# Performance work log

Measured on AMD Instinct MI355X. Metric: run time of the kernel, lower is better.

Reference implementation:

```python
import jax, jax.numpy as jnp
import numpy as np

VOCAB = 32000
EMBED = 512
HIDDEN = 512
SEQ = 4096


def setup_inputs() -> dict:
    key = jax.random.key(0)
    ks = jax.random.split(key, 20)
    s = 1.0 / np.sqrt(HIDDEN)

    def n(k, shape):
        return (jax.random.normal(k, shape, dtype=jnp.float32) * s).astype(jnp.float32)

    inp = {}
    inp["input"] = jax.random.randint(ks[0], (SEQ,), 0, VOCAB)
    inp["embed_w"] = n(ks[1], (VOCAB, EMBED))
    # layer 0 (input size EMBED), forward and backward directions; gate order i,f,g,o
    inp["Wih0f"] = n(ks[2], (4 * HIDDEN, EMBED))
    inp["Whh0f"] = n(ks[3], (4 * HIDDEN, HIDDEN))
    inp["b0f"] = n(ks[4], (4 * HIDDEN,))  # b_ih + b_hh combined (same math)
    inp["Wih0b"] = n(ks[5], (4 * HIDDEN, EMBED))
    inp["Whh0b"] = n(ks[6], (4 * HIDDEN, HIDDEN))
    inp["b0b"] = n(ks[7], (4 * HIDDEN,))
    # layer 1 (input size 2*HIDDEN)
    inp["Wih1f"] = n(ks[8], (4 * HIDDEN, 2 * HIDDEN))
    inp["Whh1f"] = n(ks[9], (4 * HIDDEN, HIDDEN))
    inp["b1f"] = n(ks[10], (4 * HIDDEN,))
    inp["Wih1b"] = n(ks[11], (4 * HIDDEN, 2 * HIDDEN))
    inp["Whh1b"] = n(ks[12], (4 * HIDDEN, HIDDEN))
    inp["b1b"] = n(ks[13], (4 * HIDDEN,))
    # output head
    inp["Wlin"] = n(ks[14], (VOCAB, 2 * HIDDEN))
    inp["blin"] = n(ks[15], (VOCAB,))
    return inp


def _lstm_dir(xproj, Whh, reverse):
    # xproj: [S, 4H] = x @ Wih.T + b, precomputed outside the scan.
    H = Whh.shape[1]
    WhhT = Whh.T  # [H, 4H]

    def step(carry, xp):
        h, c = carry
        g = xp + h @ WhhT  # [4H]
        i, f, gg, o = jnp.split(g, 4)
        i = jax.nn.sigmoid(i)
        f = jax.nn.sigmoid(f)
        gg = jnp.tanh(gg)
        o = jax.nn.sigmoid(o)
        c = f * c + i * gg
        h = o * jnp.tanh(c)
        return (h, c), h

    h0 = jnp.zeros((H,), xproj.dtype)
    _, hs = jax.lax.scan(step, (h0, h0), xproj, reverse=reverse)
    return hs  # [S, H], aligned to original time order


def _bilstm_layer(x, Wihf, Whhf, bf, Wihb, Whhb, bb):
    hf = _lstm_dir(x @ Wihf.T + bf, Whhf, reverse=False)
    hb = _lstm_dir(x @ Wihb.T + bb, Whhb, reverse=True)
    return jnp.concatenate([hf, hb], axis=-1)  # [S, 2H]


def reference(input, embed_w, Wih0f, Whh0f, b0f, Wih0b, Whh0b, b0b,
              Wih1f, Whh1f, b1f, Wih1b, Whh1b, b1b, Wlin, blin):
    x = embed_w[input]  # [S, E]  (batch=1 squeezed away; same math)
    x = _bilstm_layer(x, Wih0f, Whh0f, b0f, Wih0b, Whh0b, b0b)
    x = _bilstm_layer(x, Wih1f, Whh1f, b1f, Wih1b, Whh1b, b1b)
    out = x @ Wlin.T + blin  # [S, VOCAB]
    return out
```

## Files before the change

kernel.cpp:

```cpp
#include <hip/hip_runtime.h>
#include <hip/hip_bf16.h>
#include <stdint.h>

#define S_LEN 4096

typedef __attribute__((ext_vector_type(8))) short short8;
typedef __attribute__((ext_vector_type(8))) unsigned short ushort8;
typedef __attribute__((ext_vector_type(4))) float f32x4;
typedef __attribute__((ext_vector_type(2))) float f32x2;

__device__ inline unsigned short f2bf(float f) {
  unsigned int x = __float_as_uint(f);
  x += 0x7fffu + ((x >> 16) & 1u);
  return (unsigned short)(x >> 16);
}
__device__ inline float bf2f(unsigned short u) {
  return __uint_as_float(((unsigned int)u) << 16);
}

__device__ inline float sigm(float x) { return 1.0f / (1.0f + __expf(-x)); }
__device__ inline float tanhf_(float x) {
  float e = __expf(-2.0f * fabsf(x));
  float t = (1.0f - e) / (1.0f + e);
  return copysignf(t, x);
}

__device__ inline void gload_lds16(const void* g, void* l) {
  __builtin_amdgcn_global_load_lds(
      (const __attribute__((address_space(1))) unsigned int*)g,
      (__attribute__((address_space(3))) unsigned int*)l, 16, 0, 0);
}

__global__ void embed_kernel(const int* __restrict__ idx, const float* __restrict__ E,
                             unsigned short* __restrict__ x0b) {
  const int row = blockIdx.x;
  const int t = threadIdx.x;
  const int id = idx[row];
  f32x4 v = ((const f32x4*)(E + (size_t)id * 512))[t];
  ushort4 u;
  u.x = f2bf(v[0]); u.y = f2bf(v[1]); u.z = f2bf(v[2]); u.w = f2bf(v[3]);
  ((ushort4*)(x0b + (size_t)row * 512))[t] = u;
}

__global__ void f32_to_bf16_kernel(const float* __restrict__ src, unsigned short* __restrict__ dst) {
  const size_t i = (size_t)blockIdx.x * blockDim.x + threadIdx.x;
  f32x4 v = ((const f32x4*)src)[i];
  ushort4 u;
  u.x = f2bf(v[0]); u.y = f2bf(v[1]); u.z = f2bf(v[2]); u.w = f2bf(v[3]);
  ((ushort4*)dst)[i] = u;
}

template <bool BF32>
__global__ __launch_bounds__(256) void gemm_bt(
    const unsigned short* __restrict__ A,
    const void* __restrict__ Bsrc,
    const float* __restrict__ bias,
    float* __restrict__ C,
    int M, int N, int K)
{
  __shared__ unsigned short Al[128 * 32];
  __shared__ unsigned short Bl[128 * 32];
  const int tiles_n = N >> 7;
  const int tm = (blockIdx.x / tiles_n) << 7;
  const int tn = (blockIdx.x % tiles_n) << 7;
  const int t = threadIdx.x;
  const int w = t >> 6, l = t & 63;
  const int wr = w >> 1, wc = w & 1;

  f32x4 acc[4][4] = {};

  for (int k0 = 0; k0 < K; k0 += 32) {
    __syncthreads();
    {
      const int rb = w * 32;
      const unsigned short* ga = A + (size_t)(tm + rb + (l >> 2)) * K + k0 + (l & 3) * 8;
      gload_lds16(ga, &Al[rb * 32]);
      gload_lds16(ga + (size_t)16 * K, &Al[(rb + 16) * 32]);
    }
    if constexpr (!BF32) {
      const unsigned short* B = (const unsigned short*)Bsrc;
      const int rb = w * 32;
      const unsigned short* gb = B + (size_t)(tn + rb + (l >> 2)) * K + k0 + (l & 3) * 8;
      gload_lds16(gb, &Bl[rb * 32]);
      gload_lds16(gb + (size_t)16 * K, &Bl[(rb + 16) * 32]);
    } else {
      const float* B = (const float*)Bsrc;
      const int row = t >> 1, half = t & 1;
      const f32x4* src = (const f32x4*)(B + (size_t)(tn + row) * K + k0 + half * 16);
      f32x4 v0 = src[0], v1 = src[1], v2 = src[2], v3 = src[3];
      short8 p0, p1;
      p0[0] = f2bf(v0[0]); p0[1] = f2bf(v0[1]); p0[2] = f2bf(v0[2]); p0[3] = f2bf(v0[3]);
      p0[4] = f2bf(v1[0]); p0[5] = f2bf(v1[1]); p0[6] = f2bf(v1[2]); p0[7] = f2bf(v1[3]);
      p1[0] = f2bf(v2[0]); p1[1] = f2bf(v2[1]); p1[2] = f2bf(v2[2]); p1[3] = f2bf(v2[3]);
      p1[4] = f2bf(v3[0]); p1[5] = f2bf(v3[1]); p1[6] = f2bf(v3[2]); p1[7] = f2bf(v3[3]);
      *(short8*)&Bl[row * 32 + half * 16] = p0;
      *(short8*)&Bl[row * 32 + half * 16 + 8] = p1;
    }
    __syncthreads();

    const int lrow = l & 15;
    const int lkb = (l >> 4) * 8;
    short8 af[4], bfr[4];
    #pragma unroll
    for (int fm = 0; fm < 4; fm++)
      af[fm] = *(const short8*)&Al[(wr * 64 + fm * 16 + lrow) * 32 + lkb];
    #pragma unroll
    for (int fn = 0; fn < 4; fn++)
      bfr[fn] = *(const short8*)&Bl[(wc * 64 + fn * 16 + lrow) * 32 + lkb];
    #pragma unroll
    for (int fm = 0; fm < 4; fm++)
      #pragma unroll
      for (int fn = 0; fn < 4; fn++)
        acc[fm][fn] = __builtin_amdgcn_mfma_f32_16x16x32_bf16(af[fm], bfr[fn], acc[fm][fn], 0, 0, 0);
  }

  const int r0 = tm + wr * 64;
  const int c0 = tn + wc * 64 + (l & 15);
  const int rbase = (l >> 4) * 4;
  #pragma unroll
  for (int fm = 0; fm < 4; fm++) {
    #pragma unroll
    for (int fn = 0; fn < 4; fn++) {
      const int col = c0 + fn * 16;
      const float bv = bias ? bias[col] : 0.0f;
      #pragma unroll
      for (int rg = 0; rg < 4; rg++) {
        const int rr = r0 + fm * 16 + rbase + rg;
        C[(size_t)rr * N + col] = acc[fm][fn][rg] + bv;
      }
    }
  }
}

__global__ __launch_bounds__(512, 1) void lstm_layer(
    const unsigned short* __restrict__ WhhBf16F,
    const unsigned short* __restrict__ WhhBf16B,
    const float* __restrict__ biasF, const float* __restrict__ biasB,
    const float* __restrict__ xproj,
    unsigned int* __restrict__ Hx,
    unsigned short* __restrict__ Hb)
{
  const int S = S_LEN;
  const int dir = blockIdx.x & 1;
  const int chunk = blockIdx.x >> 1;
  const unsigned short* Whh = dir ? WhhBf16B : WhhBf16F;
  const float* bias = dir ? biasB : biasF;
  const int t = threadIdx.x;
  const int w = t >> 6, l = t & 63;
  const int g = l >> 4;
  const int jl = (l >> 3) & 1;
  const int o = l & 7;
  const int elem = w * 2 + jl;
  const int r = g * 512 + chunk * 16 + elem;
  const int xoff = dir * 2048, hoff = dir * 512;

  const ushort8* wp = (const ushort8*)(Whh + (size_t)r * 512 + o * 64);
  const float bv = bias[r];

  __shared__ float hsh[2][8 * 68];
  float c = 0.0f;
  const int slot2 = (t >> 5) * 68 + ((2 * t) & 63);

  float xp_cur = 0.0f;
  if (o == 0) {
    const int t0 = dir ? (S - 1) : 0;
    xp_cur = xproj[(size_t)t0 * 4096 + xoff + r] + bv;
  }

  for (int st = 0; st < S; st++) {
    const int tcur = dir ? (S - 1 - st) : st;
    const int pp = st & 1;

    ushort8 wv[8];
    #pragma unroll
    for (int j = 0; j < 8; j++) wv[j] = wp[j];

    float xp_nxt = 0.0f;
    if (o == 0 && st + 1 < S) {
      const int tn = dir ? (S - 2 - st) : (st + 1);
      xp_nxt = xproj[(size_t)tn * 4096 + xoff + r] + bv;
    }

    if (st == 0) {
      if (t < 256) *(f32x2*)&hsh[0][slot2] = f32x2{0.0f, 0.0f};
    } else if (t < 256) {
      const int tprev = dir ? (tcur + 1) : (tcur - 1);
      const unsigned long long* src =
          (const unsigned long long*)(Hx + (size_t)tprev * 1024 + hoff) + t;
      unsigned long long v;
      int cap = 1 << 16;
      do {
        v = __hip_atomic_load(src, __ATOMIC_RELAXED, __HIP_MEMORY_SCOPE_AGENT);
      } while (((v >> 32) == 0xFFFFFFFFull || (v & 0xFFFFFFFFull) == 0xFFFFFFFFull)
               && --cap > 0);
      *(f32x2*)&hsh[pp][slot2] =
          f32x2{__uint_as_float((unsigned int)v), __uint_as_float((unsigned int)(v >> 32))};
    }
    __syncthreads();

    float acc = 0.0f;
    const float* hb = &hsh[pp][o * 68];
    #pragma unroll
    for (int i = 0; i < 16; i++) {
      f32x4 h4 = *(const f32x4*)&hb[4 * i];
      const int j = i >> 1, hf = (i & 1) * 4;
      acc = fmaf(bf2f(wv[j][hf + 0]), h4[0], acc);
      acc = fmaf(bf2f(wv[j][hf + 1]), h4[1], acc);
      acc = fmaf(bf2f(wv[j][hf + 2]), h4[2], acc);
      acc = fmaf(bf2f(wv[j][hf + 3]), h4[3], acc);
    }
    acc += __shfl_xor(acc, 1);
    acc += __shfl_xor(acc, 2);
    acc += __shfl_xor(acc, 4);
    acc += xp_cur;

    const float av = (g == 2) ? tanhf_(acc) : sigm(acc);
    const float f_ = __shfl(av, (l & 8) + 16);
    const float g_ = __shfl(av, (l & 8) + 32);
    const float o_ = __shfl(av, (l & 8) + 48);

    c = f_ * c + av * g_;
    const float h = o_ * tanhf_(c);
    const float hpair = __shfl(h, 8);

    if (l == 0) {
      const size_t eofs = (size_t)tcur * 1024 + hoff + chunk * 16 + 2 * w;
      const unsigned long long pk =
          (unsigned long long)__float_as_uint(h) |
          ((unsigned long long)__float_as_uint(hpair) << 32);
      __hip_atomic_store((unsigned long long*)(Hx + eofs), pk,
                         __ATOMIC_RELAXED, __HIP_MEMORY_SCOPE_AGENT);
      const unsigned int hb2 = (unsigned int)f2bf(h) | ((unsigned int)f2bf(hpair) << 16);
      *(unsigned int*)(Hb + eofs) = hb2;
    }
    xp_cur = xp_nxt;
  }
}

extern "C" void kernel_launch(void* const* d_in, const int* in_sizes, int n_in,
                              void* d_out, int out_size, void* d_ws, size_t ws_size,
                              hipStream_t stream) {
  (void)in_sizes; (void)n_in; (void)out_size; (void)ws_size;
  const int*   input   = (const int*)d_in[0];
  const float* embed_w = (const float*)d_in[1];
  const float* Wih0f   = (const float*)d_in[2];
  const float* Whh0f   = (const float*)d_in[3];
  const float* b0f     = (const float*)d_in[4];
  const float* Wih0b   = (const float*)d_in[5];
  const float* Whh0b   = (const float*)d_in[6];
  const float* b0b     = (const float*)d_in[7];
  const float* Wih1f   = (const float*)d_in[8];
  const float* Whh1f   = (const float*)d_in[9];
  const float* b1f     = (const float*)d_in[10];
  const float* Wih1b   = (const float*)d_in[11];
  const float* Whh1b   = (const float*)d_in[12];
  const float* b1b     = (const float*)d_in[13];
  const float* Wlin    = (const float*)d_in[14];
  const float* blin    = (const float*)d_in[15];

  char* ws = (char*)d_ws;
  unsigned short* x0b   = (unsigned short*)(ws);
  unsigned short* Wih0  = (unsigned short*)(ws + ((size_t)4  << 20));
  unsigned short* Wih1  = (unsigned short*)(ws + ((size_t)8  << 20));
  unsigned short* H0b   = (unsigned short*)(ws + ((size_t)16 << 20));
  unsigned short* H1b   = (unsigned short*)(ws + ((size_t)24 << 20));

  float* dout  = (float*)d_out;
  float* xproj = dout;
  unsigned int* H0 = (unsigned int*)(dout + ((size_t)16 << 20));
  unsigned int* H1 = (unsigned int*)(dout + ((size_t)20 << 20));
  unsigned short* WhhB = (unsigned short*)(dout + ((size_t)24 << 20));
  unsigned short* Whh0fb = WhhB;
  unsigned short* Whh0bb = WhhB + ((size_t)1 << 20);
  unsigned short* Whh1fb = WhhB + ((size_t)2 << 20);
  unsigned short* Whh1bb = WhhB + ((size_t)3 << 20);

  hipMemsetAsync(H0, 0xFF, (size_t)8 * 1024 * 1024 * 4, stream);

  embed_kernel<<<4096, 128, 0, stream>>>(input, embed_w, x0b);

  f32_to_bf16_kernel<<<1024, 256, 0, stream>>>(Wih0f, Wih0);
  f32_to_bf16_kernel<<<1024, 256, 0, stream>>>(Wih0b, Wih0 + (size_t)2048 * 512);
  f32_to_bf16_kernel<<<2048, 256, 0, stream>>>(Wih1f, Wih1);
  f32_to_bf16_kernel<<<2048, 256, 0, stream>>>(Wih1b, Wih1 + (size_t)2048 * 1024);
  f32_to_bf16_kernel<<<1024, 256, 0, stream>>>(Whh0f, Whh0fb);
  f32_to_bf16_kernel<<<1024, 256, 0, stream>>>(Whh0b, Whh0bb);
  f32_to_bf16_kernel<<<1024, 256, 0, stream>>>(Whh1f, Whh1fb);
  f32_to_bf16_kernel<<<1024, 256, 0, stream>>>(Whh1b, Whh1bb);

  gemm_bt<false><<<32 * 32, 256, 0, stream>>>(x0b, Wih0, nullptr, xproj, 4096, 4096, 512);
  lstm_layer<<<64, 512, 0, stream>>>(Whh0fb, Whh0bb, b0f, b0b, xproj, H0, H0b);

  gemm_bt<false><<<32 * 32, 256, 0, stream>>>(H0b, Wih1, nullptr, xproj, 4096, 4096, 1024);
  lstm_layer<<<64, 512, 0, stream>>>(Whh1fb, Whh1bb, b1f, b1b, xproj, H1, H1b);

  gemm_bt<true><<<32 * 250, 256, 0, stream>>>(H1b, Wlin, blin, dout, 4096, 32000, 1024);
}
```

Measured before the change: 12.38 ms.

## Halve recurrent grid to 32 blocks with 4-lane dot-product split per gate row

Each LSTM block now handles 32 hidden elements instead of 16, with each gate row's dot product split across 4 lanes of 128 elements instead of 8 lanes of 64. This halves the number of blocks participating in the per-step cross-block handoff, reducing synchronization fan-in. Each thread now loads twice as many weights per step and runs a longer FMA chain, which raises register pressure and per-step compute latency. The spin-wait loop also keeps two outstanding loads to shorten polling latency.

```diff
diff --git a/kernel.cpp b/kernel.cpp
--- a/kernel.cpp
+++ b/kernel.cpp
@@ -147,22 +147,22 @@
   const float* bias = dir ? biasB : biasF;
   const int t = threadIdx.x;
   const int w = t >> 6, l = t & 63;
-  const int g = l >> 4;
-  const int jl = (l >> 3) & 1;
-  const int o = l & 7;
-  const int elem = w * 2 + jl;
-  const int r = g * 512 + chunk * 16 + elem;
+  const int q  = l & 3;
+  const int es = (l >> 2) & 3;
+  const int g  = l >> 4;
+  const int e  = w * 4 + es;
+  const int r  = g * 512 + chunk * 32 + e;
   const int xoff = dir * 2048, hoff = dir * 512;
 
-  const ushort8* wp = (const ushort8*)(Whh + (size_t)r * 512 + o * 64);
+  const ushort8* wp = (const ushort8*)(Whh + (size_t)r * 512 + q * 128);
   const float bv = bias[r];
 
-  __shared__ float hsh[2][8 * 68];
+  __shared__ float hsh[2][4 * 132];
   float c = 0.0f;
-  const int slot2 = (t >> 5) * 68 + ((2 * t) & 63);
+  const int slot = 132 * (t >> 6) + ((2 * t) & 127);
 
   float xp_cur = 0.0f;
-  if (o == 0) {
+  if (q == 0) {
     const int t0 = dir ? (S - 1) : 0;
     xp_cur = xproj[(size_t)t0 * 4096 + xoff + r] + bv;
   }
@@ -171,37 +171,39 @@
     const int tcur = dir ? (S - 1 - st) : st;
     const int pp = st & 1;
 
-    ushort8 wv[8];
-    #pragma unroll
-    for (int j = 0; j < 8; j++) wv[j] = wp[j];
+    ushort8 wv[16];
+    #pragma unroll
+    for (int j = 0; j < 16; j++) wv[j] = wp[j];
 
     float xp_nxt = 0.0f;
-    if (o == 0 && st + 1 < S) {
+    if (q == 0 && st + 1 < S) {
       const int tn = dir ? (S - 2 - st) : (st + 1);
       xp_nxt = xproj[(size_t)tn * 4096 + xoff + r] + bv;
     }
 
     if (st == 0) {
-      if (t < 256) *(f32x2*)&hsh[0][slot2] = f32x2{0.0f, 0.0f};
+      if (t < 256) *(f32x2*)&hsh[0][slot] = f32x2{0.0f, 0.0f};
     } else if (t < 256) {
       const int tprev = dir ? (tcur + 1) : (tcur - 1);
       const unsigned long long* src =
           (const unsigned long long*)(Hx + (size_t)tprev * 1024 + hoff) + t;
-      unsigned long long v;
+      unsigned long long v0 = __hip_atomic_load(src, __ATOMIC_RELAXED, __HIP_MEMORY_SCOPE_AGENT);
+      unsigned long long v1 = __hip_atomic_load(src, __ATOMIC_RELAXED, __HIP_MEMORY_SCOPE_AGENT);
       int cap = 1 << 16;
-      do {
-        v = __hip_atomic_load(src, __ATOMIC_RELAXED, __HIP_MEMORY_SCOPE_AGENT);
-      } while (((v >> 32) == 0xFFFFFFFFull || (v & 0xFFFFFFFFull) == 0xFFFFFFFFull)
-               && --cap > 0);
-      *(f32x2*)&hsh[pp][slot2] =
-          f32x2{__uint_as_float((unsigned int)v), __uint_as_float((unsigned int)(v >> 32))};
+      while (((v0 >> 32) == 0xFFFFFFFFull || (v0 & 0xFFFFFFFFull) == 0xFFFFFFFFull)
+             && --cap > 0) {
+        v0 = v1;
+        v1 = __hip_atomic_load(src, __ATOMIC_RELAXED, __HIP_MEMORY_SCOPE_AGENT);
+      }
+      *(f32x2*)&hsh[pp][slot] =
+          f32x2{__uint_as_float((unsigned int)v0), __uint_as_float((unsigned int)(v0 >> 32))};
     }
     __syncthreads();
 
     float acc = 0.0f;
-    const float* hb = &hsh[pp][o * 68];
-    #pragma unroll
-    for (int i = 0; i < 16; i++) {
+    const float* hb = &hsh[pp][q * 132];
+    #pragma unroll
+    for (int i = 0; i < 32; i++) {
       f32x4 h4 = *(const f32x4*)&hb[4 * i];
       const int j = i >> 1, hf = (i & 1) * 4;
       acc = fmaf(bf2f(wv[j][hf + 0]), h4[0], acc);
@@ -211,20 +213,19 @@
     }
     acc += __shfl_xor(acc, 1);
     acc += __shfl_xor(acc, 2);
-    acc += __shfl_xor(acc, 4);
     acc += xp_cur;
 
     const float av = (g == 2) ? tanhf_(acc) : sigm(acc);
-    const float f_ = __shfl(av, (l & 8) + 16);
-    const float g_ = __shfl(av, (l & 8) + 32);
-    const float o_ = __shfl(av, (l & 8) + 48);
+    const float f_ = __shfl(av, 16 + (l & 12));
+    const float g_ = __shfl(av, 32 + (l & 12));
+    const float o_ = __shfl(av, 48 + (l & 12));
 
     c = f_ * c + av * g_;
     const float h = o_ * tanhf_(c);
-    const float hpair = __shfl(h, 8);
-
-    if (l == 0) {
-      const size_t eofs = (size_t)tcur * 1024 + hoff + chunk * 16 + 2 * w;
+    const float hpair = __shfl(h, l | 4);
+
+    if ((l & 55) == 0) {
+      const size_t eofs = (size_t)tcur * 1024 + hoff + chunk * 32 + w * 4 + ((l >> 2) & 2);
       const unsigned long long pk =
           (unsigned long long)__float_as_uint(h) |
           ((unsigned long long)__float_as_uint(hpair) << 32);
@@ -289,10 +290,10 @@
   f32_to_bf16_kernel<<<1024, 256, 0, stream>>>(Whh1b, Whh1bb);
 
   gemm_bt<false><<<32 * 32, 256, 0, stream>>>(x0b, Wih0, nullptr, xproj, 4096, 4096, 512);
-  lstm_layer<<<64, 512, 0, stream>>>(Whh0fb, Whh0bb, b0f, b0b, xproj, H0, H0b);
+  lstm_layer<<<32, 512, 0, stream>>>(Whh0fb, Whh0bb, b0f, b0b, xproj, H0, H0b);
 
   gemm_bt<false><<<32 * 32, 256, 0, stream>>>(H0b, Wih1, nullptr, xproj, 4096, 4096, 1024);
-  lstm_layer<<<64, 512, 0, stream>>>(Whh1fb, Whh1bb, b1f, b1b, xproj, H1, H1b);
+  lstm_layer<<<32, 512, 0, stream>>>(Whh1fb, Whh1bb, b1f, b1b, xproj, H1, H1b);
 
   gemm_bt<true><<<32 * 250, 256, 0, stream>>>(H1b, Wlin, blin, dout, 4096, 32000, 1024);
 }
```

After: 14.28 ms. 15.3% more time.
